# Optimization experiments

Measured on AMD Instinct MI355X. Metric: run time of the kernel, lower is better.

Reference implementation:

```python
import jax, jax.numpy as jnp
import numpy as np

N = 50000      # nodes
E = 800000     # edges
G = 64         # graphs in batch
H = 256        # hidden_channels
CE = 128       # coord embed dim = H//2
OTH = 6        # in_channels - 3
ED = 8         # edge_dim
EE = 128       # edge_embedding_dim
GD = 16        # global_dim
L = 3          # num_layers


def setup_inputs() -> dict:
    key = jax.random.key(0)
    ks = jax.random.split(key, 24)
    s = 0.05
    inp = {
        "x": jax.random.normal(ks[0], (N, 9), jnp.float32),
        "edge_index": jax.random.randint(ks[1], (2, E), 0, N),
        "batch": jnp.sort(jax.random.randint(ks[2], (N,), 0, G)),
        "edge_attr": jax.random.normal(ks[3], (E, ED), jnp.float32),
        "global_x": jax.random.normal(ks[4], (G, GD), jnp.float32),
        # coordinate embedder (Linear 3->128 + relu)
        "coord_W": jax.random.normal(ks[5], (3, CE), jnp.float32) * s,
        "coord_b": jnp.zeros((CE,), jnp.float32),
        # node_mlp (Linear 6->128 + relu)
        "node_W": jax.random.normal(ks[6], (OTH, CE), jnp.float32) * s,
        "node_b": jnp.zeros((CE,), jnp.float32),
        # edge processor (Linear 8->128 + relu) and projection 128->256
        "edge_W": jax.random.normal(ks[7], (ED, EE), jnp.float32) * s,
        "edge_b": jnp.zeros((EE,), jnp.float32),
        "proj_W": jax.random.normal(ks[8], (EE, H), jnp.float32) * s,
        "proj_b": jnp.zeros((H,), jnp.float32),
        # stacked GCN layer weights
        "gcn_W": jax.random.normal(ks[9], (L, H, H), jnp.float32) * s,
        "gcn_b": jnp.zeros((L, H), jnp.float32),
        # attention pooling
        "attn_w": jax.random.normal(ks[10], (H,), jnp.float32) * s,
        "attn_b": jnp.zeros((), jnp.float32),
        # global_mlp: Linear 16->256, relu, Linear 256->256
        "gmlp_W1": jax.random.normal(ks[11], (GD, H), jnp.float32) * s,
        "gmlp_b1": jnp.zeros((H,), jnp.float32),
        "gmlp_W2": jax.random.normal(ks[12], (H, H), jnp.float32) * s,
        "gmlp_b2": jnp.zeros((H,), jnp.float32),
        # fc_out: Linear 512->256, relu, Linear 256->1
        "fc_W1": jax.random.normal(ks[13], (2 * H, H), jnp.float32) * s,
        "fc_b1": jnp.zeros((H,), jnp.float32),
        "fc_W2": jax.random.normal(ks[14], (H, 1), jnp.float32) * s,
        "fc_b2": jnp.zeros((1,), jnp.float32),
    }
    return inp


def _segsum(v, idx, num):
    return jax.ops.segment_sum(v, idx, num_segments=num)


def reference(x, edge_index, batch, edge_attr, global_x,
              coord_W, coord_b, node_W, node_b, edge_W, edge_b,
              proj_W, proj_b, gcn_W, gcn_b, attn_w, attn_b,
              gmlp_W1, gmlp_b1, gmlp_W2, gmlp_b2,
              fc_W1, fc_b1, fc_W2, fc_b2):
    relu = jax.nn.relu
    # --- node embedding: coords + other features ---
    coord_emb = relu(x[:, :3] @ coord_W + coord_b)          # [N, 128]
    other_emb = relu(x[:, 3:] @ node_W + node_b)            # [N, 128]
    x_emb = jnp.concatenate([coord_emb, other_emb], axis=1)  # [N, 256]

    # --- edge embedding, aggregated to target nodes (index_add over col) ---
    edge_emb = relu(edge_attr @ edge_W + edge_b) @ proj_W + proj_b  # [E, 256]
    col0 = edge_index[1]
    node_msg = _segsum(edge_emb, col0, N)                    # [N, 256]

    # --- GCN normalization with self-loops ---
    sl = jnp.arange(N)
    row = jnp.concatenate([edge_index[0], sl])
    col = jnp.concatenate([edge_index[1], sl])
    deg = _segsum(jnp.ones_like(col, jnp.float32), col, N)   # >= 1
    dnorm = jax.lax.rsqrt(deg)
    efac = (dnorm[row] * dnorm[col])[:, None]                # [E+N, 1]

    # --- stacked GCN layers (edge messages re-added each layer, per source) ---
    for i in range(L):
        x_in = x_emb + node_msg
        h = x_in @ gcn_W[i]                                  # [N, 256]
        x_emb = _segsum(h[row] * efac, col, N) + gcn_b[i]
        if i < L - 1:
            x_emb = relu(x_emb)

    # --- attention pooling (per-graph softmax over batch index) ---
    scores = x_emb @ attn_w + attn_b                         # [N]
    m = jax.ops.segment_max(scores, batch, num_segments=G)
    e = jnp.exp(scores - m[batch])
    denom = _segsum(e, batch, G)
    attn = e / denom[batch]
    graph_emb = _segsum(x_emb * attn[:, None], batch, G)     # [G, 256]

    # --- global features + head ---
    g = relu(global_x @ gmlp_W1 + gmlp_b1) @ gmlp_W2 + gmlp_b2
    hcat = jnp.concatenate([graph_emb, g], axis=-1)          # [G, 512]
    out = relu(hcat @ fc_W1 + fc_b1) @ fc_W2 + fc_b2         # [G, 1]
    return out
```

## Files before the change

kernel.cpp:

```cpp
#include <hip/hip_runtime.h>


typedef float f32x4 __attribute__((ext_vector_type(4)));
typedef short s16x8 __attribute__((ext_vector_type(8)));

__device__ __forceinline__ unsigned short f2bf(float f) {
  union { float f; unsigned u; } v{f};
  unsigned r = v.u + 0x7fff + ((v.u >> 16) & 1);
  return (unsigned short)(r >> 16);
}
__device__ __forceinline__ float bf2f(unsigned short s) {
  union { unsigned u; float f; } v{(unsigned)s << 16};
  return v.f;
}
__device__ __forceinline__ float blo(unsigned u) {
  union { unsigned x; float f; } v{u << 16};
  return v.f;
}
__device__ __forceinline__ float bhi(unsigned u) {
  union { unsigned x; float f; } v{u & 0xffff0000u};
  return v.f;
}
__device__ __forceinline__ unsigned pk2(float a, float b) {
  return (unsigned)f2bf(a) | ((unsigned)f2bf(b) << 16);
}

__global__ void node_embed_kernel(const float* __restrict__ x,
                                  const float* __restrict__ coord_W, const float* __restrict__ coord_b,
                                  const float* __restrict__ node_W, const float* __restrict__ node_b,
                                  short* __restrict__ x0, int N) {
  int tid = threadIdx.x;
  int node = blockIdx.x * 8 + (tid >> 5);
  if (node >= N) return;
  int ch0 = (tid & 31) * 8;
  const float* xr = x + (size_t)node * 9;
  float a[8];
  if (ch0 < 128) {
    float4 b0 = *(const float4*)&coord_b[ch0];
    float4 b1 = *(const float4*)&coord_b[ch0 + 4];
    a[0]=b0.x; a[1]=b0.y; a[2]=b0.z; a[3]=b0.w; a[4]=b1.x; a[5]=b1.y; a[6]=b1.z; a[7]=b1.w;
#pragma unroll
    for (int k = 0; k < 3; k++) {
      float xv = xr[k];
      float4 w0 = *(const float4*)&coord_W[k * 128 + ch0];
      float4 w1 = *(const float4*)&coord_W[k * 128 + ch0 + 4];
      a[0] = fmaf(xv, w0.x, a[0]); a[1] = fmaf(xv, w0.y, a[1]);
      a[2] = fmaf(xv, w0.z, a[2]); a[3] = fmaf(xv, w0.w, a[3]);
      a[4] = fmaf(xv, w1.x, a[4]); a[5] = fmaf(xv, w1.y, a[5]);
      a[6] = fmaf(xv, w1.z, a[6]); a[7] = fmaf(xv, w1.w, a[7]);
    }
  } else {
    int c0 = ch0 - 128;
    float4 b0 = *(const float4*)&node_b[c0];
    float4 b1 = *(const float4*)&node_b[c0 + 4];
    a[0]=b0.x; a[1]=b0.y; a[2]=b0.z; a[3]=b0.w; a[4]=b1.x; a[5]=b1.y; a[6]=b1.z; a[7]=b1.w;
#pragma unroll
    for (int k = 0; k < 6; k++) {
      float xv = xr[3 + k];
      float4 w0 = *(const float4*)&node_W[k * 128 + c0];
      float4 w1 = *(const float4*)&node_W[k * 128 + c0 + 4];
      a[0] = fmaf(xv, w0.x, a[0]); a[1] = fmaf(xv, w0.y, a[1]);
      a[2] = fmaf(xv, w0.z, a[2]); a[3] = fmaf(xv, w0.w, a[3]);
      a[4] = fmaf(xv, w1.x, a[4]); a[5] = fmaf(xv, w1.y, a[5]);
      a[6] = fmaf(xv, w1.z, a[6]); a[7] = fmaf(xv, w1.w, a[7]);
    }
  }
  uint4 o;
  o.x = pk2(fmaxf(a[0], 0.f), fmaxf(a[1], 0.f));
  o.y = pk2(fmaxf(a[2], 0.f), fmaxf(a[3], 0.f));
  o.z = pk2(fmaxf(a[4], 0.f), fmaxf(a[5], 0.f));
  o.w = pk2(fmaxf(a[6], 0.f), fmaxf(a[7], 0.f));
  *(uint4*)&x0[(size_t)node * 256 + ch0] = o;
}

__global__ void count_kernel(const int* __restrict__ col, int* __restrict__ cnt, int E) {
  int e = blockIdx.x * 256 + threadIdx.x;
  if (e < E) atomicAdd(&cnt[col[e]], 1);
}

__global__ void breduce_kernel(const int* __restrict__ cnt, int* __restrict__ partials, int N) {
  __shared__ int red[256];
  int t = threadIdx.x;
  int i = blockIdx.x * 256 + t;
  int v = (i < N) ? cnt[i] : 0;
  red[t] = v;
  __syncthreads();
  for (int off = 128; off; off >>= 1) {
    if (t < off) red[t] += red[t + off];
    __syncthreads();
  }
  if (t == 0) partials[blockIdx.x] = red[0];
}

__global__ void scan_partials_kernel(int* __restrict__ partials, int nb) {
  __shared__ int s[1024];
  int t = threadIdx.x;
  for (int i = t; i < nb; i += 256) s[i] = partials[i];
  __syncthreads();
  if (t == 0) {
    int run = 0;
    for (int i = 0; i < nb; i++) { int c = s[i]; s[i] = run; run += c; }
  }
  __syncthreads();
  for (int i = t; i < nb; i += 256) partials[i] = s[i];
}

__global__ void scan_apply_kernel(const int* __restrict__ cnt, const int* __restrict__ partials,
                                  int* __restrict__ rowstart, float* __restrict__ dnorm,
                                  int* __restrict__ cursor, int N) {
  __shared__ int red[256];
  int t = threadIdx.x;
  int i = blockIdx.x * 256 + t;
  int v = (i < N) ? cnt[i] : 0;
  red[t] = v;
  __syncthreads();
  for (int off = 1; off < 256; off <<= 1) {
    int x = (t >= off) ? red[t - off] : 0;
    __syncthreads();
    red[t] += x;
    __syncthreads();
  }
  if (i < N) {
    int ex = red[t] - v + partials[blockIdx.x];
    rowstart[i] = ex;
    dnorm[i] = rsqrtf((float)(v + 1));
    cursor[i] = 0;
    if (i == N - 1) rowstart[N] = ex + v;
  }
}

__global__ void scatter_kernel(const int* __restrict__ row, const int* __restrict__ col,
                               const int* __restrict__ rowstart, int* __restrict__ cursor,
                               const float* __restrict__ dnorm,
                               int2* __restrict__ pk8, int* __restrict__ eids, int E) {
  int e = blockIdx.x * 256 + threadIdx.x;
  if (e >= E) return;
  int c = col[e], r = row[e];
  int p = atomicAdd(&cursor[c], 1);
  int slot = rowstart[c] + p;
  pk8[slot] = make_int2(r, __float_as_int(dnorm[r] * dnorm[c]));
  eids[slot] = e;
}

__global__ void wt_kernel(const float* __restrict__ gcn_W, const float* __restrict__ proj_W,
                          short* __restrict__ gcnWt, short* __restrict__ projWt) {
  int idx = blockIdx.x * 256 + threadIdx.x;
  if (idx < 3 * 65536) {
    int l = idx >> 16, r = idx & 65535, n = r >> 8, k = r & 255;
    gcnWt[idx] = (short)f2bf(gcn_W[l * 65536 + k * 256 + n]);
  } else {
    int j = idx - 3 * 65536;
    int n = j >> 7, k = j & 127;
    projWt[j] = (short)f2bf(proj_W[k * 256 + n]);
  }
}

__global__ void __launch_bounds__(256) edge_msg_kernel(
    const float* __restrict__ edge_attr, const int* __restrict__ eids,
    const int* __restrict__ rowstart,
    const float* __restrict__ edge_W, const float* __restrict__ edge_b,
    unsigned* __restrict__ msg128u, int N) {
  int lane = threadIdx.x & 63;
  int node = blockIdx.x * 4 + (threadIdx.x >> 6);
  if (node >= N) return;
  int ch0 = lane * 2;
  float wa[8], wb[8];
#pragma unroll
  for (int k = 0; k < 8; k++) {
    float2 w = *(const float2*)&edge_W[k * 128 + ch0];
    wa[k] = w.x; wb[k] = w.y;
  }
  float2 bb = *(const float2*)&edge_b[ch0];
  float acc0 = 0.f, acc1 = 0.f;
  int s = rowstart[node], s1 = rowstart[node + 1];
  const float4* ea4 = (const float4*)edge_attr;
  for (; s + 4 <= s1; s += 4) {
    int e0 = eids[s], e1 = eids[s + 1], e2 = eids[s + 2], e3 = eids[s + 3];
    float4 a00 = ea4[(size_t)e0 * 2], a01 = ea4[(size_t)e0 * 2 + 1];
    float4 a10 = ea4[(size_t)e1 * 2], a11 = ea4[(size_t)e1 * 2 + 1];
    float4 a20 = ea4[(size_t)e2 * 2], a21 = ea4[(size_t)e2 * 2 + 1];
    float4 a30 = ea4[(size_t)e3 * 2], a31 = ea4[(size_t)e3 * 2 + 1];
    float t0, t1;
#define EMLP(lo, hi)                                                        \
    t0 = bb.x; t1 = bb.y;                                                   \
    t0 = fmaf(lo.x, wa[0], t0); t1 = fmaf(lo.x, wb[0], t1);                 \
    t0 = fmaf(lo.y, wa[1], t0); t1 = fmaf(lo.y, wb[1], t1);                 \
    t0 = fmaf(lo.z, wa[2], t0); t1 = fmaf(lo.z, wb[2], t1);                 \
    t0 = fmaf(lo.w, wa[3], t0); t1 = fmaf(lo.w, wb[3], t1);                 \
    t0 = fmaf(hi.x, wa[4], t0); t1 = fmaf(hi.x, wb[4], t1);                 \
    t0 = fmaf(hi.y, wa[5], t0); t1 = fmaf(hi.y, wb[5], t1);                 \
    t0 = fmaf(hi.z, wa[6], t0); t1 = fmaf(hi.z, wb[6], t1);                 \
    t0 = fmaf(hi.w, wa[7], t0); t1 = fmaf(hi.w, wb[7], t1);                 \
    acc0 += fmaxf(t0, 0.f); acc1 += fmaxf(t1, 0.f);
    EMLP(a00, a01)
    EMLP(a10, a11)
    EMLP(a20, a21)
    EMLP(a30, a31)
  }
  for (; s < s1; s++) {
    int e = eids[s];
    float4 lo = ea4[(size_t)e * 2], hi = ea4[(size_t)e * 2 + 1];
    float t0, t1;
    EMLP(lo, hi)
  }
#undef EMLP
  msg128u[(size_t)node * 64 + lane] = pk2(acc0, acc1);
}

__global__ void __launch_bounds__(256) proj_gemm_mfma(
    const short* __restrict__ msg128, const short* __restrict__ projWt,
    const float* __restrict__ proj_b, const int* __restrict__ cnt,
    short* __restrict__ node_msg, int N) {
  __shared__ short As[64][136];
  __shared__ short Bs[64][136];
  int tid = threadIdx.x;
  int n0 = blockIdx.x * 64;
  for (int i = tid; i < 64 * 32; i += 256) {
    int r = i >> 5, c4 = (i & 31) << 2;
    int n = n0 + r;
    uint2 v = make_uint2(0, 0);
    if (n < N) v = *(const uint2*)&msg128[(size_t)n * 128 + c4];
    *(uint2*)&As[r][c4] = v;
  }
  __syncthreads();
  int wave = tid >> 6, lane = tid & 63;
  int mrow = wave * 16 + (lane & 15);
  int brow = lane & 15;
  int kgrp = (lane >> 4) * 8;
  s16x8 areg[4];
#pragma unroll
  for (int kk = 0; kk < 4; kk++) areg[kk] = *(const s16x8*)&As[mrow][kk * 32 + kgrp];
  int orow0 = wave * 16 + (lane >> 4) * 4;
  int ocol = lane & 15;
  float cn[4];
#pragma unroll
  for (int r = 0; r < 4; r++) {
    int n = n0 + orow0 + r;
    cn[r] = (n < N) ? (float)cnt[n] : 0.f;
  }
  for (int cb = 0; cb < 4; cb++) {
    __syncthreads();
    for (int i = tid; i < 64 * 32; i += 256) {
      int r = i >> 5, c4 = (i & 31) << 2;
      *(uint2*)&Bs[r][c4] = *(const uint2*)&projWt[(size_t)(cb * 64 + r) * 128 + c4];
    }
    __syncthreads();
    f32x4 acc[4];
#pragma unroll
    for (int i = 0; i < 4; i++) acc[i] = (f32x4){0.f, 0.f, 0.f, 0.f};
#pragma unroll
    for (int kk = 0; kk < 4; kk++) {
#pragma unroll
      for (int nf = 0; nf < 4; nf++) {
        s16x8 b = *(const s16x8*)&Bs[nf * 16 + brow][kk * 32 + kgrp];
        acc[nf] = __builtin_amdgcn_mfma_f32_16x16x32_bf16(areg[kk], b, acc[nf], 0, 0, 0);
      }
    }
#pragma unroll
    for (int r = 0; r < 4; r++) {
      int n = n0 + orow0 + r;
      if (n < N) {
#pragma unroll
        for (int nf = 0; nf < 4; nf++) {
          int c = cb * 64 + nf * 16 + ocol;
          node_msg[(size_t)n * 256 + c] = (short)f2bf(acc[nf][r] + cn[r] * proj_b[c]);
        }
      }
    }
  }
}

__global__ void __launch_bounds__(256) gcn_gemm_add_mfma(
    const short* __restrict__ X, const short* __restrict__ M,
    const short* __restrict__ Wt, short* __restrict__ Hout, int N) {
  __shared__ short As[64][264];
  __shared__ short Bs[64][264];
  int tid = threadIdx.x;
  int n0 = blockIdx.x * 64;
  for (int i = tid; i < 64 * 64; i += 256) {
    int r = i >> 6, c4 = (i & 63) << 2;
    int n = n0 + r;
    uint2 o = make_uint2(0, 0);
    if (n < N) {
      uint2 xv = *(const uint2*)&X[(size_t)n * 256 + c4];
      uint2 mv = *(const uint2*)&M[(size_t)n * 256 + c4];
      o.x = pk2(blo(xv.x) + blo(mv.x), bhi(xv.x) + bhi(mv.x));
      o.y = pk2(blo(xv.y) + blo(mv.y), bhi(xv.y) + bhi(mv.y));
    }
    *(uint2*)&As[r][c4] = o;
  }
  __syncthreads();
  int wave = tid >> 6, lane = tid & 63;
  int mrow = wave * 16 + (lane & 15);
  int brow = lane & 15;
  int kgrp = (lane >> 4) * 8;
  s16x8 areg[8];
#pragma unroll
  for (int kk = 0; kk < 8; kk++) areg[kk] = *(const s16x8*)&As[mrow][kk * 32 + kgrp];
  int orow0 = wave * 16 + (lane >> 4) * 4;
  int ocol = lane & 15;
  for (int cb = 0; cb < 4; cb++) {
    __syncthreads();
    for (int i = tid; i < 64 * 64; i += 256) {
      int r = i >> 6, c4 = (i & 63) << 2;
      *(uint2*)&Bs[r][c4] = *(const uint2*)&Wt[(size_t)(cb * 64 + r) * 256 + c4];
    }
    __syncthreads();
    f32x4 acc[4];
#pragma unroll
    for (int i = 0; i < 4; i++) acc[i] = (f32x4){0.f, 0.f, 0.f, 0.f};
#pragma unroll
    for (int kk = 0; kk < 8; kk++) {
#pragma unroll
      for (int nf = 0; nf < 4; nf++) {
        s16x8 b = *(const s16x8*)&Bs[nf * 16 + brow][kk * 32 + kgrp];
        acc[nf] = __builtin_amdgcn_mfma_f32_16x16x32_bf16(areg[kk], b, acc[nf], 0, 0, 0);
      }
    }
#pragma unroll
    for (int nf = 0; nf < 4; nf++) {
#pragma unroll
      for (int r = 0; r < 4; r++) {
        int n = n0 + orow0 + r;
        if (n < N) Hout[(size_t)n * 256 + cb * 64 + nf * 16 + ocol] = (short)f2bf(acc[nf][r]);
      }
    }
  }
}

__global__ void __launch_bounds__(256) gcn_gemm_mfma(
    const short* __restrict__ Xin, const short* __restrict__ Wt,
    short* __restrict__ Hout, int N) {
  __shared__ short As[64][264];
  __shared__ short Bs[64][264];
  int tid = threadIdx.x;
  int n0 = blockIdx.x * 64;
  for (int i = tid; i < 64 * 64; i += 256) {
    int r = i >> 6, c4 = (i & 63) << 2;
    int n = n0 + r;
    uint2 v = make_uint2(0, 0);
    if (n < N) v = *(const uint2*)&Xin[(size_t)n * 256 + c4];
    *(uint2*)&As[r][c4] = v;
  }
  __syncthreads();
  int wave = tid >> 6, lane = tid & 63;
  int mrow = wave * 16 + (lane & 15);
  int brow = lane & 15;
  int kgrp = (lane >> 4) * 8;
  s16x8 areg[8];
#pragma unroll
  for (int kk = 0; kk < 8; kk++) areg[kk] = *(const s16x8*)&As[mrow][kk * 32 + kgrp];
  int orow0 = wave * 16 + (lane >> 4) * 4;
  int ocol = lane & 15;
  for (int cb = 0; cb < 4; cb++) {
    __syncthreads();
    for (int i = tid; i < 64 * 64; i += 256) {
      int r = i >> 6, c4 = (i & 63) << 2;
      *(uint2*)&Bs[r][c4] = *(const uint2*)&Wt[(size_t)(cb * 64 + r) * 256 + c4];
    }
    __syncthreads();
    f32x4 acc[4];
#pragma unroll
    for (int i = 0; i < 4; i++) acc[i] = (f32x4){0.f, 0.f, 0.f, 0.f};
#pragma unroll
    for (int kk = 0; kk < 8; kk++) {
#pragma unroll
      for (int nf = 0; nf < 4; nf++) {
        s16x8 b = *(const s16x8*)&Bs[nf * 16 + brow][kk * 32 + kgrp];
        acc[nf] = __builtin_amdgcn_mfma_f32_16x16x32_bf16(areg[kk], b, acc[nf], 0, 0, 0);
      }
    }
#pragma unroll
    for (int nf = 0; nf < 4; nf++) {
#pragma unroll
      for (int r = 0; r < 4; r++) {
        int n = n0 + orow0 + r;
        if (n < N) Hout[(size_t)n * 256 + cb * 64 + nf * 16 + ocol] = (short)f2bf(acc[nf][r]);
      }
    }
  }
}

__global__ void __launch_bounds__(256) gcn_agg_kernel(
    const short* __restrict__ h, const int2* __restrict__ pk8,
    const int* __restrict__ rowstart, const float* __restrict__ dnorm,
    const float* __restrict__ b, const short* __restrict__ node_msg,
    short* __restrict__ xin, int N) {
  int lane = threadIdx.x & 63;
  int node = blockIdx.x * 4 + (threadIdx.x >> 6);
  if (node >= N) return;
  int ch0 = lane << 2;
  size_t rowb = (size_t)node * 256 + ch0;
  float dn = dnorm[node];
  float wgt = dn * dn;
  uint2 hv = *(const uint2*)&h[rowb];
  float a0 = blo(hv.x) * wgt, a1 = bhi(hv.x) * wgt;
  float a2 = blo(hv.y) * wgt, a3 = bhi(hv.y) * wgt;
  int s = rowstart[node], s1 = rowstart[node + 1];
  for (; s + 4 <= s1; s += 4) {
    int2 p0 = pk8[s], p1 = pk8[s + 1], p2 = pk8[s + 2], p3 = pk8[s + 3];
    float f0 = __int_as_float(p0.y), f1 = __int_as_float(p1.y);
    float f2 = __int_as_float(p2.y), f3 = __int_as_float(p3.y);
    uint2 v0 = *(const uint2*)&h[(size_t)p0.x * 256 + ch0];
    uint2 v1 = *(const uint2*)&h[(size_t)p1.x * 256 + ch0];
    uint2 v2 = *(const uint2*)&h[(size_t)p2.x * 256 + ch0];
    uint2 v3 = *(const uint2*)&h[(size_t)p3.x * 256 + ch0];
    a0 = fmaf(blo(v0.x), f0, a0); a1 = fmaf(bhi(v0.x), f0, a1);
    a2 = fmaf(blo(v0.y), f0, a2); a3 = fmaf(bhi(v0.y), f0, a3);
    a0 = fmaf(blo(v1.x), f1, a0); a1 = fmaf(bhi(v1.x), f1, a1);
    a2 = fmaf(blo(v1.y), f1, a2); a3 = fmaf(bhi(v1.y), f1, a3);
    a0 = fmaf(blo(v2.x), f2, a0); a1 = fmaf(bhi(v2.x), f2, a1);
    a2 = fmaf(blo(v2.y), f2, a2); a3 = fmaf(bhi(v2.y), f2, a3);
    a0 = fmaf(blo(v3.x), f3, a0); a1 = fmaf(bhi(v3.x), f3, a1);
    a2 = fmaf(blo(v3.y), f3, a2); a3 = fmaf(bhi(v3.y), f3, a3);
  }
  for (; s < s1; s++) {
    int2 p = pk8[s];
    float f = __int_as_float(p.y);
    uint2 v = *(const uint2*)&h[(size_t)p.x * 256 + ch0];
    a0 = fmaf(blo(v.x), f, a0); a1 = fmaf(bhi(v.x), f, a1);
    a2 = fmaf(blo(v.y), f, a2); a3 = fmaf(bhi(v.y), f, a3);
  }
  float4 bv = *(const float4*)&b[ch0];
  uint2 mv = *(const uint2*)&node_msg[rowb];
  float y0 = fmaxf(a0 + bv.x, 0.f) + blo(mv.x);
  float y1 = fmaxf(a1 + bv.y, 0.f) + bhi(mv.x);
  float y2 = fmaxf(a2 + bv.z, 0.f) + blo(mv.y);
  float y3 = fmaxf(a3 + bv.w, 0.f) + bhi(mv.y);
  uint2 o;
  o.x = pk2(y0, y1);
  o.y = pk2(y2, y3);
  *(uint2*)&xin[rowb] = o;
}

__global__ void __launch_bounds__(256) final_agg_kernel(
    const short* __restrict__ h, const int2* __restrict__ pk8,
    const int* __restrict__ rowstart, const float* __restrict__ dnorm,
    const float* __restrict__ b, short* __restrict__ x_emb,
    const float* __restrict__ attn_w, const float* __restrict__ attn_b,
    float* __restrict__ scores, int N) {
  int lane = threadIdx.x & 63;
  int node = blockIdx.x * 4 + (threadIdx.x >> 6);
  if (node >= N) return;
  int ch0 = lane << 2;
  size_t rowb = (size_t)node * 256 + ch0;
  float dn = dnorm[node];
  float wgt = dn * dn;
  uint2 hv = *(const uint2*)&h[rowb];
  float a0 = blo(hv.x) * wgt, a1 = bhi(hv.x) * wgt;
  float a2 = blo(hv.y) * wgt, a3 = bhi(hv.y) * wgt;
  int s = rowstart[node], s1 = rowstart[node + 1];
  for (; s + 4 <= s1; s += 4) {
    int2 p0 = pk8[s], p1 = pk8[s + 1], p2 = pk8[s + 2], p3 = pk8[s + 3];
    float f0 = __int_as_float(p0.y), f1 = __int_as_float(p1.y);
    float f2 = __int_as_float(p2.y), f3 = __int_as_float(p3.y);
    uint2 v0 = *(const uint2*)&h[(size_t)p0.x * 256 + ch0];
    uint2 v1 = *(const uint2*)&h[(size_t)p1.x * 256 + ch0];
    uint2 v2 = *(const uint2*)&h[(size_t)p2.x * 256 + ch0];
    uint2 v3 = *(const uint2*)&h[(size_t)p3.x * 256 + ch0];
    a0 = fmaf(blo(v0.x), f0, a0); a1 = fmaf(bhi(v0.x), f0, a1);
    a2 = fmaf(blo(v0.y), f0, a2); a3 = fmaf(bhi(v0.y), f0, a3);
    a0 = fmaf(blo(v1.x), f1, a0); a1 = fmaf(bhi(v1.x), f1, a1);
    a2 = fmaf(blo(v1.y), f1, a2); a3 = fmaf(bhi(v1.y), f1, a3);
    a0 = fmaf(blo(v2.x), f2, a0); a1 = fmaf(bhi(v2.x), f2, a1);
    a2 = fmaf(blo(v2.y), f2, a2); a3 = fmaf(bhi(v2.y), f2, a3);
    a0 = fmaf(blo(v3.x), f3, a0); a1 = fmaf(bhi(v3.x), f3, a1);
    a2 = fmaf(blo(v3.y), f3, a2); a3 = fmaf(bhi(v3.y), f3, a3);
  }
  for (; s < s1; s++) {
    int2 p = pk8[s];
    float f = __int_as_float(p.y);
    uint2 v = *(const uint2*)&h[(size_t)p.x * 256 + ch0];
    a0 = fmaf(blo(v.x), f, a0); a1 = fmaf(bhi(v.x), f, a1);
    a2 = fmaf(blo(v.y), f, a2); a3 = fmaf(bhi(v.y), f, a3);
  }
  float4 bv = *(const float4*)&b[ch0];
  a0 += bv.x; a1 += bv.y; a2 += bv.z; a3 += bv.w;
  uint2 o;
  o.x = pk2(a0, a1);
  o.y = pk2(a2, a3);
  *(uint2*)&x_emb[rowb] = o;
  float4 aw = *(const float4*)&attn_w[ch0];
  float p = a0 * aw.x + a1 * aw.y + a2 * aw.z + a3 * aw.w;
#pragma unroll
  for (int off = 32; off; off >>= 1) p += __shfl_down(p, off);
  if (lane == 0) scores[node] = p + attn_b[0];
}

__global__ void gse_kernel(const int* __restrict__ batch, int* __restrict__ gs,
                           int* __restrict__ ge, int N) {
  int i = blockIdx.x * 256 + threadIdx.x;
  if (i >= N) return;
  int g = batch[i];
  if (i == 0) gs[g] = 0;
  else {
    int gp = batch[i - 1];
    if (gp != g) { gs[g] = i; ge[gp] = i - 1; }
  }
  if (i == N - 1) ge[g] = N - 1;
}

__global__ void softmax_kernel(const float* __restrict__ scores, const int* __restrict__ gs,
                               const int* __restrict__ ge, float* __restrict__ wnode) {
  int g = blockIdx.x;
  int tid = threadIdx.x;
  __shared__ float red[256];
  int s0 = gs[g], e1 = ge[g];
  if (s0 > e1) return;
  int s1 = e1 + 1;
  float m = -1e30f;
  for (int i = s0 + tid; i < s1; i += 256) m = fmaxf(m, scores[i]);
  red[tid] = m;
  __syncthreads();
  for (int off = 128; off; off >>= 1) {
    if (tid < off) red[tid] = fmaxf(red[tid], red[tid + off]);
    __syncthreads();
  }
  m = red[0];
  __syncthreads();
  float d = 0.f;
  for (int i = s0 + tid; i < s1; i += 256) d += expf(scores[i] - m);
  red[tid] = d;
  __syncthreads();
  for (int off = 128; off; off >>= 1) {
    if (tid < off) red[tid] += red[tid + off];
    __syncthreads();
  }
  float rd = 1.f / red[0];
  for (int i = s0 + tid; i < s1; i += 256) wnode[i] = expf(scores[i] - m) * rd;
}

__global__ void __launch_bounds__(256) pool_sum_kernel(
    const short* __restrict__ x_emb, const float* __restrict__ wnode,
    const int* __restrict__ batch, float* __restrict__ graph_emb, int N) {
  __shared__ int sb[256];
  __shared__ float sw[256];
  int ch = threadIdx.x;
  int i0 = blockIdx.x * 256;
  int lim = min(256, N - i0);
  if (ch < lim) { sb[ch] = batch[i0 + ch]; sw[ch] = wnode[i0 + ch]; }
  __syncthreads();
  int curg = sb[0];
  float acc = 0.f;
  for (int j = 0; j < lim; j++) {
    int g = sb[j];
    if (g != curg) {
      atomicAdd(&graph_emb[(size_t)curg * 256 + ch], acc);
      acc = 0.f;
      curg = g;
    }
    acc = fmaf(bf2f((unsigned short)x_emb[(size_t)(i0 + j) * 256 + ch]), sw[j], acc);
  }
  atomicAdd(&graph_emb[(size_t)curg * 256 + ch], acc);
}

__global__ void head_kernel(const float* __restrict__ global_x, const float* __restrict__ graph_emb,
                            const float* __restrict__ W1, const float* __restrict__ b1,
                            const float* __restrict__ W2, const float* __restrict__ b2,
                            const float* __restrict__ fW1, const float* __restrict__ fb1,
                            const float* __restrict__ fW2, const float* __restrict__ fb2,
                            float* __restrict__ out) {
  int g = blockIdx.x;
  int ch = threadIdx.x;
  __shared__ float t1[256], g2s[256], t3s[256];
  float a = b1[ch];
  const float* gx = global_x + g * 16;
#pragma unroll
  for (int k = 0; k < 16; k++) a = fmaf(gx[k], W1[k * 256 + ch], a);
  t1[ch] = fmaxf(a, 0.f);
  __syncthreads();
  float bb = b2[ch];
  for (int k = 0; k < 256; k++) bb = fmaf(t1[k], W2[k * 256 + ch], bb);
  g2s[ch] = bb;
  __syncthreads();
  float c = fb1[ch];
  const float* ger = graph_emb + (size_t)g * 256;
  for (int k = 0; k < 256; k++) c = fmaf(ger[k], fW1[k * 256 + ch], c);
  for (int k = 0; k < 256; k++) c = fmaf(g2s[k], fW1[(256 + k) * 256 + ch], c);
  t3s[ch] = fmaxf(c, 0.f);
  __syncthreads();
  t1[ch] = t3s[ch] * fW2[ch];
  __syncthreads();
  for (int off = 128; off; off >>= 1) {
    if (ch < off) t1[ch] += t1[ch + off];
    __syncthreads();
  }
  if (ch == 0) out[g] = t1[0] + fb2[0];
}

extern "C" void kernel_launch(void* const* d_in, const int* in_sizes, int n_in,
                              void* d_out, int out_size, void* d_ws, size_t ws_size,
                              hipStream_t stream) {
  const float* x        = (const float*)d_in[0];
  const int*   ei       = (const int*)d_in[1];
  const int*   batch    = (const int*)d_in[2];
  const float* edge_attr= (const float*)d_in[3];
  const float* global_x = (const float*)d_in[4];
  const float* coord_W  = (const float*)d_in[5];
  const float* coord_b  = (const float*)d_in[6];
  const float* node_W   = (const float*)d_in[7];
  const float* node_b   = (const float*)d_in[8];
  const float* edge_W   = (const float*)d_in[9];
  const float* edge_b   = (const float*)d_in[10];
  const float* proj_W   = (const float*)d_in[11];
  const float* proj_b   = (const float*)d_in[12];
  const float* gcn_W    = (const float*)d_in[13];
  const float* gcn_b    = (const float*)d_in[14];
  const float* attn_w   = (const float*)d_in[15];
  const float* attn_b   = (const float*)d_in[16];
  const float* gmlp_W1  = (const float*)d_in[17];
  const float* gmlp_b1  = (const float*)d_in[18];
  const float* gmlp_W2  = (const float*)d_in[19];
  const float* gmlp_b2  = (const float*)d_in[20];
  const float* fc_W1    = (const float*)d_in[21];
  const float* fc_b1    = (const float*)d_in[22];
  const float* fc_W2    = (const float*)d_in[23];
  const float* fc_b2    = (const float*)d_in[24];

  const int N = in_sizes[0] / 9;
  const int E = in_sizes[3] / 8;
  const int G = in_sizes[4] / 16;
  const int NB = (N + 255) / 256;
  const int NM = (N + 63) / 64;

  char* w = (char*)d_ws;
  auto alloc = [&](size_t bytes) -> char* {
    char* p = w;
    w += (bytes + 255) & ~(size_t)255;
    return p;
  };
  short* x0       = (short*)alloc((size_t)N * 256 * 2);
  short* node_msg = (short*)alloc((size_t)N * 256 * 2);
  short* hA       = (short*)alloc((size_t)N * 256 * 2);
  short* hB       = (short*)alloc((size_t)N * 256 * 2);
  short* xinBuf   = (short*)alloc((size_t)N * 256 * 2);
  short* x_emb    = (short*)alloc((size_t)N * 256 * 2);
  short* msg128   = x_emb;
  int2*  pk8      = (int2*)alloc((size_t)E * 8);
  int*   eids     = (int*)alloc((size_t)E * 4);
  short* gcnWt    = (short*)alloc((size_t)3 * 65536 * 2);
  short* projWt   = (short*)alloc((size_t)256 * 128 * 2);
  int*   cnt      = (int*)alloc((size_t)N * 4);
  int*   rowstart = (int*)alloc((size_t)(N + 1) * 4);
  int*   cursor   = (int*)alloc((size_t)N * 4);
  float* dnorm    = (float*)alloc((size_t)N * 4);
  float* scores   = (float*)alloc((size_t)N * 4);
  float* wnode    = (float*)alloc((size_t)N * 4);
  int*   partials = (int*)alloc((size_t)NB * 4);
  int*   gs       = (int*)alloc((size_t)G * 4);
  int*   ge       = (int*)alloc((size_t)G * 4);
  float* graph_emb= (float*)alloc((size_t)G * 256 * 4);

  hipMemsetAsync(cnt, 0, (size_t)N * 4, stream);
  hipMemsetAsync(gs, 0x7f, (size_t)G * 4, stream);
  hipMemsetAsync(ge, 0xff, (size_t)G * 4, stream);
  hipMemsetAsync(graph_emb, 0, (size_t)G * 256 * 4, stream);

  wt_kernel<<<(3 * 65536 + 256 * 128 + 255) / 256, 256, 0, stream>>>(gcn_W, proj_W, gcnWt, projWt);
  node_embed_kernel<<<(N + 7) / 8, 256, 0, stream>>>(
      x, coord_W, coord_b, node_W, node_b, x0, N);
  count_kernel<<<(E + 255) / 256, 256, 0, stream>>>(ei + E, cnt, E);
  breduce_kernel<<<NB, 256, 0, stream>>>(cnt, partials, N);
  scan_partials_kernel<<<1, 256, 0, stream>>>(partials, NB);
  scan_apply_kernel<<<NB, 256, 0, stream>>>(cnt, partials, rowstart, dnorm, cursor, N);
  scatter_kernel<<<(E + 255) / 256, 256, 0, stream>>>(
      ei, ei + E, rowstart, cursor, dnorm, pk8, eids, E);
  edge_msg_kernel<<<(N + 3) / 4, 256, 0, stream>>>(
      edge_attr, eids, rowstart, edge_W, edge_b, (unsigned*)msg128, N);
  proj_gemm_mfma<<<NM, 256, 0, stream>>>(
      msg128, projWt, proj_b, cnt, node_msg, N);
  gcn_gemm_add_mfma<<<NM, 256, 0, stream>>>(
      x0, node_msg, gcnWt, hA, N);
  gcn_agg_kernel<<<(N + 3) / 4, 256, 0, stream>>>(
      hA, pk8, rowstart, dnorm, gcn_b, node_msg, xinBuf, N);
  gcn_gemm_mfma<<<NM, 256, 0, stream>>>(
      xinBuf, gcnWt + 65536, hB, N);
  gcn_agg_kernel<<<(N + 3) / 4, 256, 0, stream>>>(
      hB, pk8, rowstart, dnorm, gcn_b + 256, node_msg, xinBuf, N);
  gcn_gemm_mfma<<<NM, 256, 0, stream>>>(
      xinBuf, gcnWt + 2 * 65536, hA, N);
  final_agg_kernel<<<(N + 3) / 4, 256, 0, stream>>>(
      hA, pk8, rowstart, dnorm, gcn_b + 512, x_emb, attn_w, attn_b, scores, N);
  gse_kernel<<<(N + 255) / 256, 256, 0, stream>>>(batch, gs, ge, N);
  softmax_kernel<<<G, 256, 0, stream>>>(scores, gs, ge, wnode);
  pool_sum_kernel<<<NB, 256, 0, stream>>>(x_emb, wnode, batch, graph_emb, N);
  head_kernel<<<G, 256, 0, stream>>>(global_x, graph_emb, gmlp_W1, gmlp_b1, gmlp_W2, gmlp_b2,
                                     fc_W1, fc_b1, fc_W2, fc_b2, (float*)d_out);
}
```

Baseline: 819.6 us.

## Fuse node embedding into first GCN GEMM, merge graph-bounds into scan, unroll gathers

```diff
diff --git a/kernel.cpp b/kernel.cpp
--- a/kernel.cpp
+++ b/kernel.cpp
@@ -23,54 +23,6 @@
 }
 __device__ __forceinline__ unsigned pk2(float a, float b) {
   return (unsigned)f2bf(a) | ((unsigned)f2bf(b) << 16);
-}
-
-__global__ void node_embed_kernel(const float* __restrict__ x,
-                                  const float* __restrict__ coord_W, const float* __restrict__ coord_b,
-                                  const float* __restrict__ node_W, const float* __restrict__ node_b,
-                                  short* __restrict__ x0, int N) {
-  int tid = threadIdx.x;
-  int node = blockIdx.x * 8 + (tid >> 5);
-  if (node >= N) return;
-  int ch0 = (tid & 31) * 8;
-  const float* xr = x + (size_t)node * 9;
-  float a[8];
-  if (ch0 < 128) {
-    float4 b0 = *(const float4*)&coord_b[ch0];
-    float4 b1 = *(const float4*)&coord_b[ch0 + 4];
-    a[0]=b0.x; a[1]=b0.y; a[2]=b0.z; a[3]=b0.w; a[4]=b1.x; a[5]=b1.y; a[6]=b1.z; a[7]=b1.w;
-#pragma unroll
-    for (int k = 0; k < 3; k++) {
-      float xv = xr[k];
-      float4 w0 = *(const float4*)&coord_W[k * 128 + ch0];
-      float4 w1 = *(const float4*)&coord_W[k * 128 + ch0 + 4];
-      a[0] = fmaf(xv, w0.x, a[0]); a[1] = fmaf(xv, w0.y, a[1]);
-      a[2] = fmaf(xv, w0.z, a[2]); a[3] = fmaf(xv, w0.w, a[3]);
-      a[4] = fmaf(xv, w1.x, a[4]); a[5] = fmaf(xv, w1.y, a[5]);
-      a[6] = fmaf(xv, w1.z, a[6]); a[7] = fmaf(xv, w1.w, a[7]);
-    }
-  } else {
-    int c0 = ch0 - 128;
-    float4 b0 = *(const float4*)&node_b[c0];
-    float4 b1 = *(const float4*)&node_b[c0 + 4];
-    a[0]=b0.x; a[1]=b0.y; a[2]=b0.z; a[3]=b0.w; a[4]=b1.x; a[5]=b1.y; a[6]=b1.z; a[7]=b1.w;
-#pragma unroll
-    for (int k = 0; k < 6; k++) {
-      float xv = xr[3 + k];
-      float4 w0 = *(const float4*)&node_W[k * 128 + c0];
-      float4 w1 = *(const float4*)&node_W[k * 128 + c0 + 4];
-      a[0] = fmaf(xv, w0.x, a[0]); a[1] = fmaf(xv, w0.y, a[1]);
-      a[2] = fmaf(xv, w0.z, a[2]); a[3] = fmaf(xv, w0.w, a[3]);
-      a[4] = fmaf(xv, w1.x, a[4]); a[5] = fmaf(xv, w1.y, a[5]);
-      a[6] = fmaf(xv, w1.z, a[6]); a[7] = fmaf(xv, w1.w, a[7]);
-    }
-  }
-  uint4 o;
-  o.x = pk2(fmaxf(a[0], 0.f), fmaxf(a[1], 0.f));
-  o.y = pk2(fmaxf(a[2], 0.f), fmaxf(a[3], 0.f));
-  o.z = pk2(fmaxf(a[4], 0.f), fmaxf(a[5], 0.f));
-  o.w = pk2(fmaxf(a[6], 0.f), fmaxf(a[7], 0.f));
-  *(uint4*)&x0[(size_t)node * 256 + ch0] = o;
 }
 
 __global__ void count_kernel(const int* __restrict__ col, int* __restrict__ cnt, int E) {
@@ -107,7 +59,9 @@
 
 __global__ void scan_apply_kernel(const int* __restrict__ cnt, const int* __restrict__ partials,
                                   int* __restrict__ rowstart, float* __restrict__ dnorm,
-                                  int* __restrict__ cursor, int N) {
+                                  int* __restrict__ cursor,
+                                  const int* __restrict__ batch, int* __restrict__ gs,
+                                  int* __restrict__ ge, int N) {
   __shared__ int red[256];
   int t = threadIdx.x;
   int i = blockIdx.x * 256 + t;
@@ -126,6 +80,13 @@
     dnorm[i] = rsqrtf((float)(v + 1));
     cursor[i] = 0;
     if (i == N - 1) rowstart[N] = ex + v;
+    int g = batch[i];
+    if (i == 0) gs[g] = 0;
+    else {
+      int gp = batch[i - 1];
+      if (gp != g) { gs[g] = i; ge[gp] = i - 1; }
+    }
+    if (i == N - 1) ge[g] = N - 1;
   }
 }
 
@@ -174,13 +135,7 @@
   float acc0 = 0.f, acc1 = 0.f;
   int s = rowstart[node], s1 = rowstart[node + 1];
   const float4* ea4 = (const float4*)edge_attr;
-  for (; s + 4 <= s1; s += 4) {
-    int e0 = eids[s], e1 = eids[s + 1], e2 = eids[s + 2], e3 = eids[s + 3];
-    float4 a00 = ea4[(size_t)e0 * 2], a01 = ea4[(size_t)e0 * 2 + 1];
-    float4 a10 = ea4[(size_t)e1 * 2], a11 = ea4[(size_t)e1 * 2 + 1];
-    float4 a20 = ea4[(size_t)e2 * 2], a21 = ea4[(size_t)e2 * 2 + 1];
-    float4 a30 = ea4[(size_t)e3 * 2], a31 = ea4[(size_t)e3 * 2 + 1];
-    float t0, t1;
+  float t0, t1;
 #define EMLP(lo, hi)                                                        \
     t0 = bb.x; t1 = bb.y;                                                   \
     t0 = fmaf(lo.x, wa[0], t0); t1 = fmaf(lo.x, wb[0], t1);                 \
@@ -192,15 +147,31 @@
     t0 = fmaf(hi.z, wa[6], t0); t1 = fmaf(hi.z, wb[6], t1);                 \
     t0 = fmaf(hi.w, wa[7], t0); t1 = fmaf(hi.w, wb[7], t1);                 \
     acc0 += fmaxf(t0, 0.f); acc1 += fmaxf(t1, 0.f);
-    EMLP(a00, a01)
-    EMLP(a10, a11)
-    EMLP(a20, a21)
-    EMLP(a30, a31)
+  for (; s + 8 <= s1; s += 8) {
+    int e0 = eids[s],     e1 = eids[s + 1], e2 = eids[s + 2], e3 = eids[s + 3];
+    int e4 = eids[s + 4], e5 = eids[s + 5], e6 = eids[s + 6], e7 = eids[s + 7];
+    float4 a00 = ea4[(size_t)e0 * 2], a01 = ea4[(size_t)e0 * 2 + 1];
+    float4 a10 = ea4[(size_t)e1 * 2], a11 = ea4[(size_t)e1 * 2 + 1];
+    float4 a20 = ea4[(size_t)e2 * 2], a21 = ea4[(size_t)e2 * 2 + 1];
+    float4 a30 = ea4[(size_t)e3 * 2], a31 = ea4[(size_t)e3 * 2 + 1];
+    float4 a40 = ea4[(size_t)e4 * 2], a41 = ea4[(size_t)e4 * 2 + 1];
+    float4 a50 = ea4[(size_t)e5 * 2], a51 = ea4[(size_t)e5 * 2 + 1];
+    float4 a60 = ea4[(size_t)e6 * 2], a61 = ea4[(size_t)e6 * 2 + 1];
+    float4 a70 = ea4[(size_t)e7 * 2], a71 = ea4[(size_t)e7 * 2 + 1];
+    EMLP(a00, a01) EMLP(a10, a11) EMLP(a20, a21) EMLP(a30, a31)
+    EMLP(a40, a41) EMLP(a50, a51) EMLP(a60, a61) EMLP(a70, a71)
+  }
+  for (; s + 4 <= s1; s += 4) {
+    int e0 = eids[s], e1 = eids[s + 1], e2 = eids[s + 2], e3 = eids[s + 3];
+    float4 a00 = ea4[(size_t)e0 * 2], a01 = ea4[(size_t)e0 * 2 + 1];
+    float4 a10 = ea4[(size_t)e1 * 2], a11 = ea4[(size_t)e1 * 2 + 1];
+    float4 a20 = ea4[(size_t)e2 * 2], a21 = ea4[(size_t)e2 * 2 + 1];
+    float4 a30 = ea4[(size_t)e3 * 2], a31 = ea4[(size_t)e3 * 2 + 1];
+    EMLP(a00, a01) EMLP(a10, a11) EMLP(a20, a21) EMLP(a30, a31)
   }
   for (; s < s1; s++) {
     int e = eids[s];
     float4 lo = ea4[(size_t)e * 2], hi = ea4[(size_t)e * 2 + 1];
-    float t0, t1;
     EMLP(lo, hi)
   }
 #undef EMLP
@@ -270,9 +241,12 @@
   }
 }
 
-__global__ void __launch_bounds__(256) gcn_gemm_add_mfma(
-    const short* __restrict__ X, const short* __restrict__ M,
-    const short* __restrict__ Wt, short* __restrict__ Hout, int N) {
+__global__ void __launch_bounds__(256) gcn_gemm_embed_mfma(
+    const float* __restrict__ x,
+    const float* __restrict__ coord_W, const float* __restrict__ coord_b,
+    const float* __restrict__ node_W, const float* __restrict__ node_b,
+    const short* __restrict__ M, const short* __restrict__ Wt,
+    short* __restrict__ Hout, int N) {
   __shared__ short As[64][264];
   __shared__ short Bs[64][264];
   int tid = threadIdx.x;
@@ -282,10 +256,33 @@
     int n = n0 + r;
     uint2 o = make_uint2(0, 0);
     if (n < N) {
-      uint2 xv = *(const uint2*)&X[(size_t)n * 256 + c4];
+      const float* xr = x + (size_t)n * 9;
+      float e0, e1, e2, e3;
+      if (c4 < 128) {
+        float4 bb = *(const float4*)&coord_b[c4];
+        e0 = bb.x; e1 = bb.y; e2 = bb.z; e3 = bb.w;
+#pragma unroll
+        for (int k = 0; k < 3; k++) {
+          float xv = xr[k];
+          float4 w = *(const float4*)&coord_W[k * 128 + c4];
+          e0 = fmaf(xv, w.x, e0); e1 = fmaf(xv, w.y, e1);
+          e2 = fmaf(xv, w.z, e2); e3 = fmaf(xv, w.w, e3);
+        }
+      } else {
+        int c0 = c4 - 128;
+        float4 bb = *(const float4*)&node_b[c0];
+        e0 = bb.x; e1 = bb.y; e2 = bb.z; e3 = bb.w;
+#pragma unroll
+        for (int k = 0; k < 6; k++) {
+          float xv = xr[3 + k];
+          float4 w = *(const float4*)&node_W[k * 128 + c0];
+          e0 = fmaf(xv, w.x, e0); e1 = fmaf(xv, w.y, e1);
+          e2 = fmaf(xv, w.z, e2); e3 = fmaf(xv, w.w, e3);
+        }
+      }
       uint2 mv = *(const uint2*)&M[(size_t)n * 256 + c4];
-      o.x = pk2(blo(xv.x) + blo(mv.x), bhi(xv.x) + bhi(mv.x));
-      o.y = pk2(blo(xv.y) + blo(mv.y), bhi(xv.y) + bhi(mv.y));
+      o.x = pk2(fmaxf(e0, 0.f) + blo(mv.x), fmaxf(e1, 0.f) + bhi(mv.x));
+      o.y = pk2(fmaxf(e2, 0.f) + blo(mv.y), fmaxf(e3, 0.f) + bhi(mv.y));
     }
     *(uint2*)&As[r][c4] = o;
   }
@@ -380,6 +377,11 @@
     }
   }
 }
+
+#define AGG_STEP(p, v)                                                      \
+  { float f = __int_as_float(p.y);                                          \
+    a0 = fmaf(blo(v.x), f, a0); a1 = fmaf(bhi(v.x), f, a1);                 \
+    a2 = fmaf(blo(v.y), f, a2); a3 = fmaf(bhi(v.y), f, a3); }
 
 __global__ void __launch_bounds__(256) gcn_agg_kernel(
     const short* __restrict__ h, const int2* __restrict__ pk8,
@@ -397,29 +399,32 @@
   float a0 = blo(hv.x) * wgt, a1 = bhi(hv.x) * wgt;
   float a2 = blo(hv.y) * wgt, a3 = bhi(hv.y) * wgt;
   int s = rowstart[node], s1 = rowstart[node + 1];
-  for (; s + 4 <= s1; s += 4) {
-    int2 p0 = pk8[s], p1 = pk8[s + 1], p2 = pk8[s + 2], p3 = pk8[s + 3];
-    float f0 = __int_as_float(p0.y), f1 = __int_as_float(p1.y);
-    float f2 = __int_as_float(p2.y), f3 = __int_as_float(p3.y);
+  for (; s + 8 <= s1; s += 8) {
+    int2 p0 = pk8[s],     p1 = pk8[s + 1], p2 = pk8[s + 2], p3 = pk8[s + 3];
+    int2 p4 = pk8[s + 4], p5 = pk8[s + 5], p6 = pk8[s + 6], p7 = pk8[s + 7];
     uint2 v0 = *(const uint2*)&h[(size_t)p0.x * 256 + ch0];
     uint2 v1 = *(const uint2*)&h[(size_t)p1.x * 256 + ch0];
     uint2 v2 = *(const uint2*)&h[(size_t)p2.x * 256 + ch0];
     uint2 v3 = *(const uint2*)&h[(size_t)p3.x * 256 + ch0];
-    a0 = fmaf(blo(v0.x), f0, a0); a1 = fmaf(bhi(v0.x), f0, a1);
-    a2 = fmaf(blo(v0.y), f0, a2); a3 = fmaf(bhi(v0.y), f0, a3);
-    a0 = fmaf(blo(v1.x), f1, a0); a1 = fmaf(bhi(v1.x), f1, a1);
-    a2 = fmaf(blo(v1.y), f1, a2); a3 = fmaf(bhi(v1.y), f1, a3);
-    a0 = fmaf(blo(v2.x), f2, a0); a1 = fmaf(bhi(v2.x), f2, a1);
-    a2 = fmaf(blo(v2.y), f2, a2); a3 = fmaf(bhi(v2.y), f2, a3);
-    a0 = fmaf(blo(v3.x), f3, a0); a1 = fmaf(bhi(v3.x), f3, a1);
-    a2 = fmaf(blo(v3.y), f3, a2); a3 = fmaf(bhi(v3.y), f3, a3);
+    uint2 v4 = *(const uint2*)&h[(size_t)p4.x * 256 + ch0];
+    uint2 v5 = *(const uint2*)&h[(size_t)p5.x * 256 + ch0];
+    uint2 v6 = *(const uint2*)&h[(size_t)p6.x * 256 + ch0];
+    uint2 v7 = *(const uint2*)&h[(size_t)p7.x * 256 + ch0];
+    AGG_STEP(p0, v0) AGG_STEP(p1, v1) AGG_STEP(p2, v2) AGG_STEP(p3, v3)
+    AGG_STEP(p4, v4) AGG_STEP(p5, v5) AGG_STEP(p6, v6) AGG_STEP(p7, v7)
+  }
+  for (; s + 4 <= s1; s += 4) {
+    int2 p0 = pk8[s], p1 = pk8[s + 1], p2 = pk8[s + 2], p3 = pk8[s + 3];
+    uint2 v0 = *(const uint2*)&h[(size_t)p0.x * 256 + ch0];
+    uint2 v1 = *(const uint2*)&h[(size_t)p1.x * 256 + ch0];
+    uint2 v2 = *(const uint2*)&h[(size_t)p2.x * 256 + ch0];
+    uint2 v3 = *(const uint2*)&h[(size_t)p3.x * 256 + ch0];
+    AGG_STEP(p0, v0) AGG_STEP(p1, v1) AGG_STEP(p2, v2) AGG_STEP(p3, v3)
   }
   for (; s < s1; s++) {
     int2 p = pk8[s];
-    float f = __int_as_float(p.y);
     uint2 v = *(const uint2*)&h[(size_t)p.x * 256 + ch0];
-    a0 = fmaf(blo(v.x), f, a0); a1 = fmaf(bhi(v.x), f, a1);
-    a2 = fmaf(blo(v.y), f, a2); a3 = fmaf(bhi(v.y), f, a3);
+    AGG_STEP(p, v)
   }
   float4 bv = *(const float4*)&b[ch0];
   uint2 mv = *(const uint2*)&node_msg[rowb];
@@ -450,29 +455,32 @@
   float a0 = blo(hv.x) * wgt, a1 = bhi(hv.x) * wgt;
   float a2 = blo(hv.y) * wgt, a3 = bhi(hv.y) * wgt;
   int s = rowstart[node], s1 = rowstart[node + 1];
-  for (; s + 4 <= s1; s += 4) {
-    int2 p0 = pk8[s], p1 = pk8[s + 1], p2 = pk8[s + 2], p3 = pk8[s + 3];
-    float f0 = __int_as_float(p0.y), f1 = __int_as_float(p1.y);
-    float f2 = __int_as_float(p2.y), f3 = __int_as_float(p3.y);
+  for (; s + 8 <= s1; s += 8) {
+    int2 p0 = pk8[s],     p1 = pk8[s + 1], p2 = pk8[s + 2], p3 = pk8[s + 3];
+    int2 p4 = pk8[s + 4], p5 = pk8[s + 5], p6 = pk8[s + 6], p7 = pk8[s + 7];
     uint2 v0 = *(const uint2*)&h[(size_t)p0.x * 256 + ch0];
     uint2 v1 = *(const uint2*)&h[(size_t)p1.x * 256 + ch0];
     uint2 v2 = *(const uint2*)&h[(size_t)p2.x * 256 + ch0];
     uint2 v3 = *(const uint2*)&h[(size_t)p3.x * 256 + ch0];
-    a0 = fmaf(blo(v0.x), f0, a0); a1 = fmaf(bhi(v0.x), f0, a1);
-    a2 = fmaf(blo(v0.y), f0, a2); a3 = fmaf(bhi(v0.y), f0, a3);
-    a0 = fmaf(blo(v1.x), f1, a0); a1 = fmaf(bhi(v1.x), f1, a1);
-    a2 = fmaf(blo(v1.y), f1, a2); a3 = fmaf(bhi(v1.y), f1, a3);
-    a0 = fmaf(blo(v2.x), f2, a0); a1 = fmaf(bhi(v2.x), f2, a1);
-    a2 = fmaf(blo(v2.y), f2, a2); a3 = fmaf(bhi(v2.y), f2, a3);
-    a0 = fmaf(blo(v3.x), f3, a0); a1 = fmaf(bhi(v3.x), f3, a1);
-    a2 = fmaf(blo(v3.y), f3, a2); a3 = fmaf(bhi(v3.y), f3, a3);
+    uint2 v4 = *(const uint2*)&h[(size_t)p4.x * 256 + ch0];
+    uint2 v5 = *(const uint2*)&h[(size_t)p5.x * 256 + ch0];
+    uint2 v6 = *(const uint2*)&h[(size_t)p6.x * 256 + ch0];
+    uint2 v7 = *(const uint2*)&h[(size_t)p7.x * 256 + ch0];
+    AGG_STEP(p0, v0) AGG_STEP(p1, v1) AGG_STEP(p2, v2) AGG_STEP(p3, v3)
+    AGG_STEP(p4, v4) AGG_STEP(p5, v5) AGG_STEP(p6, v6) AGG_STEP(p7, v7)
+  }
+  for (; s + 4 <= s1; s += 4) {
+    int2 p0 = pk8[s], p1 = pk8[s + 1], p2 = pk8[s + 2], p3 = pk8[s + 3];
+    uint2 v0 = *(const uint2*)&h[(size_t)p0.x * 256 + ch0];
+    uint2 v1 = *(const uint2*)&h[(size_t)p1.x * 256 + ch0];
+    uint2 v2 = *(const uint2*)&h[(size_t)p2.x * 256 + ch0];
+    uint2 v3 = *(const uint2*)&h[(size_t)p3.x * 256 + ch0];
+    AGG_STEP(p0, v0) AGG_STEP(p1, v1) AGG_STEP(p2, v2) AGG_STEP(p3, v3)
   }
   for (; s < s1; s++) {
     int2 p = pk8[s];
-    float f = __int_as_float(p.y);
     uint2 v = *(const uint2*)&h[(size_t)p.x * 256 + ch0];
-    a0 = fmaf(blo(v.x), f, a0); a1 = fmaf(bhi(v.x), f, a1);
-    a2 = fmaf(blo(v.y), f, a2); a3 = fmaf(bhi(v.y), f, a3);
+    AGG_STEP(p, v)
   }
   float4 bv = *(const float4*)&b[ch0];
   a0 += bv.x; a1 += bv.y; a2 += bv.z; a3 += bv.w;
@@ -486,19 +494,7 @@
   for (int off = 32; off; off >>= 1) p += __shfl_down(p, off);
   if (lane == 0) scores[node] = p + attn_b[0];
 }
-
-__global__ void gse_kernel(const int* __restrict__ batch, int* __restrict__ gs,
-                           int* __restrict__ ge, int N) {
-  int i = blockIdx.x * 256 + threadIdx.x;
-  if (i >= N) return;
-  int g = batch[i];
-  if (i == 0) gs[g] = 0;
-  else {
-    int gp = batch[i - 1];
-    if (gp != g) { gs[g] = i; ge[gp] = i - 1; }
-  }
-  if (i == N - 1) ge[g] = N - 1;
-}
+#undef AGG_STEP
 
 __global__ void softmax_kernel(const float* __restrict__ scores, const int* __restrict__ gs,
                                const int* __restrict__ ge, float* __restrict__ wnode) {
@@ -629,7 +625,6 @@
     w += (bytes + 255) & ~(size_t)255;
     return p;
   };
-  short* x0       = (short*)alloc((size_t)N * 256 * 2);
   short* node_msg = (short*)alloc((size_t)N * 256 * 2);
   short* hA       = (short*)alloc((size_t)N * 256 * 2);
   short* hB       = (short*)alloc((size_t)N * 256 * 2);
@@ -657,20 +652,19 @@
   hipMemsetAsync(graph_emb, 0, (size_t)G * 256 * 4, stream);
 
   wt_kernel<<<(3 * 65536 + 256 * 128 + 255) / 256, 256, 0, stream>>>(gcn_W, proj_W, gcnWt, projWt);
-  node_embed_kernel<<<(N + 7) / 8, 256, 0, stream>>>(
-      x, coord_W, coord_b, node_W, node_b, x0, N);
   count_kernel<<<(E + 255) / 256, 256, 0, stream>>>(ei + E, cnt, E);
   breduce_kernel<<<NB, 256, 0, stream>>>(cnt, partials, N);
   scan_partials_kernel<<<1, 256, 0, stream>>>(partials, NB);
-  scan_apply_kernel<<<NB, 256, 0, stream>>>(cnt, partials, rowstart, dnorm, cursor, N);
+  scan_apply_kernel<<<NB, 256, 0, stream>>>(cnt, partials, rowstart, dnorm, cursor,
+                                            batch, gs, ge, N);
   scatter_kernel<<<(E + 255) / 256, 256, 0, stream>>>(
       ei, ei + E, rowstart, cursor, dnorm, pk8, eids, E);
   edge_msg_kernel<<<(N + 3) / 4, 256, 0, stream>>>(
       edge_attr, eids, rowstart, edge_W, edge_b, (unsigned*)msg128, N);
   proj_gemm_mfma<<<NM, 256, 0, stream>>>(
       msg128, projWt, proj_b, cnt, node_msg, N);
-  gcn_gemm_add_mfma<<<NM, 256, 0, stream>>>(
-      x0, node_msg, gcnWt, hA, N);
+  gcn_gemm_embed_mfma<<<NM, 256, 0, stream>>>(
+      x, coord_W, coord_b, node_W, node_b, node_msg, gcnWt, hA, N);
   gcn_agg_kernel<<<(N + 3) / 4, 256, 0, stream>>>(
       hA, pk8, rowstart, dnorm, gcn_b, node_msg, xinBuf, N);
   gcn_gemm_mfma<<<NM, 256, 0, stream>>>(
@@ -681,7 +675,6 @@
       xinBuf, gcnWt + 2 * 65536, hA, N);
   final_agg_kernel<<<(N + 3) / 4, 256, 0, stream>>>(
       hA, pk8, rowstart, dnorm, gcn_b + 512, x_emb, attn_w, attn_b, scores, N);
-  gse_kernel<<<(N + 255) / 256, 256, 0, stream>>>(batch, gs, ge, N);
   softmax_kernel<<<G, 256, 0, stream>>>(scores, gs, ge, wnode);
   pool_sum_kernel<<<NB, 256, 0, stream>>>(x_emb, wnode, batch, graph_emb, N);
   head_kernel<<<G, 256, 0, stream>>>(global_x, graph_emb, gmlp_W1, gmlp_b1, gmlp_W2, gmlp_b2,
```

After: 788.1 us. 1.04x faster.
